# Kernel optimization log

Hardware: AMD Instinct MI355X
Metric: run time of the kernel (lower is better)

Reference implementation:

```python
import jax, jax.numpy as jnp
import numpy as np

B, T, E, H, L = 8, 4096, 1024, 16, 64  # batch, seq, embed, heads, local window
HD = E // H


def setup_inputs() -> dict:
    key = jax.random.key(0)
    ks = jax.random.split(key, 5)
    s = 1.0 / np.sqrt(E).astype(np.float32)
    x = jax.random.normal(ks[0], (B, T, E), dtype=jnp.float32)
    W_qkv = jax.random.normal(ks[1], (3 * E, E), dtype=jnp.float32) * s
    b_qkv = jnp.zeros((3 * E,), dtype=jnp.float32)
    W_out = jax.random.normal(ks[2], (E, E), dtype=jnp.float32) * s
    b_out = jnp.zeros((E,), dtype=jnp.float32)
    return {"x": x, "W_qkv": W_qkv, "b_qkv": b_qkv, "W_out": W_out, "b_out": b_out}


def reference(x, W_qkv, b_qkv, W_out, b_out):
    b, t, e = x.shape
    scaling = HD ** (-0.5)
    # T is already a multiple of L, so need_pad = 0 (matches torch path)
    qkv = x @ W_qkv.T + b_qkv                      # (B,T,3E)
    q, k, v = jnp.split(qkv, 3, axis=-1)           # each (B,T,E)
    q = q * scaling

    def to_blocks(a):
        # (B,T,E) -> (B,H,T/L,L,HD); matches torch view/transpose sequence
        return a.reshape(b, t, H, HD).transpose(0, 2, 1, 3).reshape(b, H, t // L, L, HD)

    qb, kb, vb = to_blocks(q), to_blocks(k), to_blocks(v)
    attn = jax.nn.softmax(jnp.einsum('bhnld,bhnmd->bhnlm', qb, kb), axis=-1)
    out = jnp.einsum('bhnlm,bhnmd->bhnld', attn, vb)  # (B,H,N,L,HD)
    out = out.reshape(b, H, t, HD).transpose(0, 2, 1, 3).reshape(b, t, e)
    return out @ W_out.T + b_out
```

## Files before the change

### kernel.cpp

```cpp
#include <hip/hip_runtime.h>
#include <hip/hip_bf16.h>

typedef __hip_bfloat16 bf16;
typedef __attribute__((ext_vector_type(8))) short short8;
typedef __attribute__((ext_vector_type(4))) float f32x4;

__device__ __forceinline__ void gload_lds16(const void* g, void* l) {
    __builtin_amdgcn_global_load_lds(
        (const __attribute__((address_space(1))) void*)g,
        (__attribute__((address_space(3))) void*)l, 16, 0, 0);
}

__device__ __forceinline__ void store_out(bf16* p, float v)  { *p = __float2bfloat16(v); }
__device__ __forceinline__ void store_out(float* p, float v) { *p = v; }

__global__ __launch_bounds__(256)
void cvt_f32_bf16(const float* __restrict__ in, bf16* __restrict__ out, long n)
{
    const long i = ((long)blockIdx.x * 256 + threadIdx.x) * 8;
    if (i + 8 > n) return;
    float4 a = *(const float4*)(in + i);
    float4 b = *(const float4*)(in + i + 4);
    bf16 o[8];
    o[0] = __float2bfloat16(a.x); o[1] = __float2bfloat16(a.y);
    o[2] = __float2bfloat16(a.z); o[3] = __float2bfloat16(a.w);
    o[4] = __float2bfloat16(b.x); o[5] = __float2bfloat16(b.y);
    o[6] = __float2bfloat16(b.z); o[7] = __float2bfloat16(b.w);
    *(uint4*)(out + i) = *(const uint4*)o;
}

template <typename OutT>
__global__ __launch_bounds__(512, 2)
void gemm256(const bf16* __restrict__ A, const bf16* __restrict__ Bt,
             const float* __restrict__ bias, OutT* __restrict__ C,
             int N, int K, int gxt)
{
    __shared__ bf16 As[4][8192];
    __shared__ bf16 Bs[4][8192];

    const int nwg  = gridDim.x;
    const int orig = blockIdx.x;
    const int qq = nwg >> 3, rr = nwg & 7, xc = orig & 7;
    const int wg = (xc < rr ? xc * (qq + 1) : rr * (qq + 1) + (xc - rr) * qq)
                 + (orig >> 3);
    const long m0 = (long)(wg / gxt) * 256;
    const long n0 = (long)(wg % gxt) * 256;

    const int tid = threadIdx.x;
    const int wv  = tid >> 6;
    const int ln  = tid & 63;
    const int l15 = ln & 15;
    const int qd  = ln >> 4;
    const int wm  = wv >> 2, wn = wv & 3;

    const int e0 = tid * 8;
    const int r0 = e0 >> 5, c0 = e0 & 31;
    const bf16* gA0 = A  + (m0 + r0) * K + c0;
    const bf16* gA1 = A  + (m0 + 128 + r0) * K + c0;
    const bf16* gB0 = Bt + (n0 + r0) * K + c0;
    const bf16* gB1 = Bt + (n0 + 128 + r0) * K + c0;
    const int lw = wv * 512;

    const int NT = K >> 5;

#define STAGE_A(bb, src) do { \
        gload_lds16(gA0 + (src) * 32, &As[bb][lw]); \
        gload_lds16(gA1 + (src) * 32, &As[bb][4096 + lw]); } while (0)
#define STAGE_B(bb, src) do { \
        gload_lds16(gB0 + (src) * 32, &Bs[bb][lw]); \
        gload_lds16(gB1 + (src) * 32, &Bs[bb][4096 + lw]); } while (0)

    {
        const int s1 = 1 < NT ? 1 : 0;
        const int s2 = 2 < NT ? 2 : 0;
        STAGE_A(0, 0);  STAGE_B(0, 0);
        STAGE_A(1, s1); STAGE_B(1, s1);
        STAGE_A(2, s2); STAGE_B(2, s2);
    }

    f32x4 acc[8][4] = {};

    for (int kt = 0; kt < NT; ++kt) {
        const int b   = kt & 3;
        const int ks  = kt + 3;
        const int bb  = ks & 3;
        const int src = ks < NT ? ks : 0;

        asm volatile("s_waitcnt vmcnt(8)" ::: "memory");
        __builtin_amdgcn_s_barrier();
        asm volatile("" ::: "memory");

        const bf16* Ab = As[b];
        const bf16* Bb = Bs[b];

        short8 af[4], bf[4];
#pragma unroll
        for (int mi = 0; mi < 4; ++mi)
            af[mi] = *(const short8*)&Ab[(wm * 128 + mi * 16 + l15) * 32 + qd * 8];
#pragma unroll
        for (int ni = 0; ni < 4; ++ni)
            bf[ni] = *(const short8*)&Bb[(wn * 64 + ni * 16 + l15) * 32 + qd * 8];
        STAGE_A(bb, src);
        __builtin_amdgcn_s_setprio(1);
#pragma unroll
        for (int mi = 0; mi < 4; ++mi)
#pragma unroll
            for (int ni = 0; ni < 4; ++ni)
                acc[mi][ni] = __builtin_amdgcn_mfma_f32_16x16x32_bf16(
                    af[mi], bf[ni], acc[mi][ni], 0, 0, 0);
        __builtin_amdgcn_s_setprio(0);

#pragma unroll
        for (int mi = 0; mi < 4; ++mi)
            af[mi] = *(const short8*)&Ab[(wm * 128 + (mi + 4) * 16 + l15) * 32 + qd * 8];
        STAGE_B(bb, src);
        __builtin_amdgcn_s_setprio(1);
#pragma unroll
        for (int mi = 0; mi < 4; ++mi)
#pragma unroll
            for (int ni = 0; ni < 4; ++ni)
                acc[mi + 4][ni] = __builtin_amdgcn_mfma_f32_16x16x32_bf16(
                    af[mi], bf[ni], acc[mi + 4][ni], 0, 0, 0);
        __builtin_amdgcn_s_setprio(0);
    }
#undef STAGE_A
#undef STAGE_B

    const long ccol = n0 + wn * 64;
    float bsv[4];
#pragma unroll
    for (int ni = 0; ni < 4; ++ni)
        bsv[ni] = bias[ccol + ni * 16 + l15];
#pragma unroll
    for (int mi = 0; mi < 8; ++mi) {
#pragma unroll
        for (int r = 0; r < 4; ++r) {
            const long row = m0 + wm * 128 + mi * 16 + qd * 4 + r;
            OutT* cp = C + row * N + ccol + l15;
#pragma unroll
            for (int ni = 0; ni < 4; ++ni)
                store_out(cp + ni * 16, acc[mi][ni][r] + bsv[ni]);
        }
    }
}

#define LROW 72

__global__ __launch_bounds__(256)
void attn_local(const bf16* __restrict__ qkv, bf16* __restrict__ out)
{
    __shared__ bf16 Qs[64 * LROW];
    __shared__ bf16 Ks[64 * LROW];
    __shared__ bf16 Vt[64 * LROW];
    __shared__ bf16 Ps[64 * LROW];

    const int cb = blockIdx.x;
    const int h  = blockIdx.y;
    const int tid = threadIdx.x;

    const long qoff = (long)cb * 64 * 3072 + h * 64;

#pragma unroll
    for (int p = 0; p < 2; ++p) {
        const int e = (p * 256 + tid) * 8;
        const int tk = e >> 6, cl = e & 63;
        const long g = qoff + (long)tk * 3072 + cl;
        *(uint4*)&Qs[tk * LROW + cl] = *(const uint4*)&qkv[g];
        *(uint4*)&Ks[tk * LROW + cl] = *(const uint4*)&qkv[g + 1024];
        uint4 vv = *(const uint4*)&qkv[g + 2048];
        const bf16* vp = (const bf16*)&vv;
#pragma unroll
        for (int j = 0; j < 8; ++j)
            Vt[(cl + j) * LROW + tk] = vp[j];
    }
    __syncthreads();

    const int wv = tid >> 6, ln = tid & 63, l15 = ln & 15, qd = ln >> 4;

    f32x4 sacc[4] = {};
#pragma unroll
    for (int kk = 0; kk < 64; kk += 32) {
        short8 aq = *(const short8*)&Qs[(wv * 16 + l15) * LROW + kk + qd * 8];
#pragma unroll
        for (int ni = 0; ni < 4; ++ni) {
            short8 bk = *(const short8*)&Ks[(ni * 16 + l15) * LROW + kk + qd * 8];
            sacc[ni] = __builtin_amdgcn_mfma_f32_16x16x32_bf16(aq, bk, sacc[ni], 0, 0, 0);
        }
    }

    float linv[4];
#pragma unroll
    for (int r = 0; r < 4; ++r) {
        float m = -3.4e38f;
#pragma unroll
        for (int ni = 0; ni < 4; ++ni) m = fmaxf(m, sacc[ni][r]);
#pragma unroll
        for (int off = 1; off < 16; off <<= 1) m = fmaxf(m, __shfl_xor(m, off));
        float s = 0.f, pv[4];
#pragma unroll
        for (int ni = 0; ni < 4; ++ni) {
            pv[ni] = __expf(0.125f * (sacc[ni][r] - m));
            s += pv[ni];
        }
#pragma unroll
        for (int off = 1; off < 16; off <<= 1) s += __shfl_xor(s, off);
        linv[r] = 1.f / s;
        const int row = wv * 16 + qd * 4 + r;
#pragma unroll
        for (int ni = 0; ni < 4; ++ni)
            Ps[row * LROW + ni * 16 + l15] = __float2bfloat16(pv[ni]);
    }
    __syncthreads();

    f32x4 oacc[4] = {};
#pragma unroll
    for (int kk = 0; kk < 64; kk += 32) {
        short8 ap = *(const short8*)&Ps[(wv * 16 + l15) * LROW + kk + qd * 8];
#pragma unroll
        for (int ni = 0; ni < 4; ++ni) {
            short8 bv = *(const short8*)&Vt[(ni * 16 + l15) * LROW + kk + qd * 8];
            oacc[ni] = __builtin_amdgcn_mfma_f32_16x16x32_bf16(ap, bv, oacc[ni], 0, 0, 0);
        }
    }

    const long obase = (long)cb * 64 * 1024 + h * 64;
#pragma unroll
    for (int r = 0; r < 4; ++r) {
        const int row = wv * 16 + qd * 4 + r;
#pragma unroll
        for (int ni = 0; ni < 4; ++ni)
            out[obase + (long)row * 1024 + ni * 16 + l15] =
                __float2bfloat16(oacc[ni][r] * linv[r]);
    }
}

extern "C" void kernel_launch(void* const* d_in, const int* in_sizes, int n_in,
                              void* d_out, int out_size, void* d_ws, size_t ws_size,
                              hipStream_t stream) {
    const float* x     = (const float*)d_in[0];
    const float* W_qkv = (const float*)d_in[1];
    const float* b_qkv = (const float*)d_in[2];
    const float* W_out = (const float*)d_in[3];
    const float* b_out = (const float*)d_in[4];
    float* out = (float*)d_out;

    bf16* Wqkv_b = (bf16*)d_ws;
    bf16* Wout_b = Wqkv_b + (size_t)3072 * 1024;
    bf16* chunk0 = Wout_b + (size_t)1024 * 1024;
    const size_t fixed_bytes = ((size_t)3072 * 1024 + (size_t)1024 * 1024) * 2;

    static const int cands[8] = {32768, 16384, 8192, 4096, 2048, 1024, 512, 256};
    int CH = 256;
    for (int i = 0; i < 8; ++i)
        if (fixed_bytes + (size_t)cands[i] * 10240 <= ws_size) { CH = cands[i]; break; }

    bf16* xb    = chunk0;
    bf16* qkvb  = xb + (size_t)CH * 1024;
    bf16* attnb = qkvb + (size_t)CH * 3072;

    const dim3 blk(256);
    const dim3 gblk(512);

    cvt_f32_bf16<<<dim3((3072 * 1024) / 2048), blk, 0, stream>>>(W_qkv, Wqkv_b, 3072 * 1024);
    cvt_f32_bf16<<<dim3((1024 * 1024) / 2048), blk, 0, stream>>>(W_out, Wout_b, 1024 * 1024);

    const int mt = CH / 256;

    for (int c0 = 0; c0 < 32768; c0 += CH) {
        const long ne = (long)CH * 1024;
        cvt_f32_bf16<<<dim3((int)(ne / 2048)), blk, 0, stream>>>(x + (size_t)c0 * 1024, xb, ne);
        gemm256<bf16><<<dim3(mt * (3072 / 256)), gblk, 0, stream>>>(
            xb, Wqkv_b, b_qkv, qkvb, 3072, 1024, 3072 / 256);
        attn_local<<<dim3(CH / 64, 16), blk, 0, stream>>>(qkvb, attnb);
        gemm256<float><<<dim3(mt * (1024 / 256)), gblk, 0, stream>>>(
            attnb, Wout_b, b_out, out + (size_t)c0 * 1024, 1024, 1024, 1024 / 256);
    }
}
```

Before: 576.6 us.

## Restructure GEMM mainloop with 64-wide K double buffer, swizzled LDS, fine barriers

The 256x256 GEMM mainloop moves from a 4-stage ring of 32-wide K slices to a double buffer of 64-wide K tiles split into two halves. The loop is hand-scheduled into half-tile MFMA chunks separated by barriers and sched_barriers so LDS reads, async global-to-LDS loads and MFMAs interleave more tightly. An XOR swizzle on the LDS column is added to reduce bank conflicts on the fragment reads. The extra barriers and the manual schedule may add sync overhead, and K must be a multiple of 128 for the unrolled loop.

```diff
diff --git a/kernel.cpp b/kernel.cpp
--- a/kernel.cpp
+++ b/kernel.cpp
@@ -35,8 +35,8 @@
              const float* __restrict__ bias, OutT* __restrict__ C,
              int N, int K, int gxt)
 {
-    __shared__ bf16 As[4][8192];
-    __shared__ bf16 Bs[4][8192];
+    __shared__ bf16 LA[2][2][8192];
+    __shared__ bf16 LB[2][2][8192];
 
     const int nwg  = gridDim.x;
     const int orig = blockIdx.x;
@@ -53,76 +53,75 @@
     const int qd  = ln >> 4;
     const int wm  = wv >> 2, wn = wv & 3;
 
-    const int e0 = tid * 8;
-    const int r0 = e0 >> 5, c0 = e0 & 31;
-    const bf16* gA0 = A  + (m0 + r0) * K + c0;
-    const bf16* gA1 = A  + (m0 + 128 + r0) * K + c0;
-    const bf16* gB0 = Bt + (n0 + r0) * K + c0;
-    const bf16* gB1 = Bt + (n0 + 128 + r0) * K + c0;
+    const int sl = (qd ^ (l15 & 3)) << 3;
+
+    const int srow = tid >> 2;
+    const int scol = ((tid & 3) ^ ((tid >> 2) & 3)) << 3;
+    const bf16* gA0 = A  + (m0 + srow) * K + scol;
+    const bf16* gA1 = A  + (m0 + 128 + srow) * K + scol;
+    const bf16* gB0 = Bt + (n0 + srow) * K + scol;
+    const bf16* gB1 = Bt + (n0 + 128 + srow) * K + scol;
     const int lw = wv * 512;
 
-    const int NT = K >> 5;
-
-#define STAGE_A(bb, src) do { \
-        gload_lds16(gA0 + (src) * 32, &As[bb][lw]); \
-        gload_lds16(gA1 + (src) * 32, &As[bb][4096 + lw]); } while (0)
-#define STAGE_B(bb, src) do { \
-        gload_lds16(gB0 + (src) * 32, &Bs[bb][lw]); \
-        gload_lds16(gB1 + (src) * 32, &Bs[bb][4096 + lw]); } while (0)
-
-    {
-        const int s1 = 1 < NT ? 1 : 0;
-        const int s2 = 2 < NT ? 2 : 0;
-        STAGE_A(0, 0);  STAGE_B(0, 0);
-        STAGE_A(1, s1); STAGE_B(1, s1);
-        STAGE_A(2, s2); STAGE_B(2, s2);
-    }
-
-    f32x4 acc[8][4] = {};
-
-    for (int kt = 0; kt < NT; ++kt) {
-        const int b   = kt & 3;
-        const int ks  = kt + 3;
-        const int bb  = ks & 3;
-        const int src = ks < NT ? ks : 0;
-
-        asm volatile("s_waitcnt vmcnt(8)" ::: "memory");
-        __builtin_amdgcn_s_barrier();
-        asm volatile("" ::: "memory");
-
-        const bf16* Ab = As[b];
-        const bf16* Bb = Bs[b];
-
-        short8 af[4], bf[4];
-#pragma unroll
-        for (int mi = 0; mi < 4; ++mi)
-            af[mi] = *(const short8*)&Ab[(wm * 128 + mi * 16 + l15) * 32 + qd * 8];
-#pragma unroll
-        for (int ni = 0; ni < 4; ++ni)
-            bf[ni] = *(const short8*)&Bb[(wn * 64 + ni * 16 + l15) * 32 + qd * 8];
-        STAGE_A(bb, src);
-        __builtin_amdgcn_s_setprio(1);
-#pragma unroll
-        for (int mi = 0; mi < 4; ++mi)
-#pragma unroll
-            for (int ni = 0; ni < 4; ++ni)
-                acc[mi][ni] = __builtin_amdgcn_mfma_f32_16x16x32_bf16(
-                    af[mi], bf[ni], acc[mi][ni], 0, 0, 0);
-        __builtin_amdgcn_s_setprio(0);
-
-#pragma unroll
-        for (int mi = 0; mi < 4; ++mi)
-            af[mi] = *(const short8*)&Ab[(wm * 128 + (mi + 4) * 16 + l15) * 32 + qd * 8];
-        STAGE_B(bb, src);
-        __builtin_amdgcn_s_setprio(1);
-#pragma unroll
-        for (int mi = 0; mi < 4; ++mi)
-#pragma unroll
-            for (int ni = 0; ni < 4; ++ni)
-                acc[mi + 4][ni] = __builtin_amdgcn_mfma_f32_16x16x32_bf16(
-                    af[mi], bf[ni], acc[mi + 4][ni], 0, 0, 0);
-        __builtin_amdgcn_s_setprio(0);
-    }
+    const int NT = K >> 6;
+
+#define STAGE_A(DB, KH, KT) do { \
+        gload_lds16(gA0 + (KT) * 64 + (KH) * 32, &LA[DB][KH][lw]); \
+        gload_lds16(gA1 + (KT) * 64 + (KH) * 32, &LA[DB][KH][4096 + lw]); } while (0)
+#define STAGE_B(DB, KH, KT) do { \
+        gload_lds16(gB0 + (KT) * 64 + (KH) * 32, &LB[DB][KH][lw]); \
+        gload_lds16(gB1 + (KT) * 64 + (KH) * 32, &LB[DB][KH][4096 + lw]); } while (0)
+
+    STAGE_A(0, 0, 0); STAGE_B(0, 0, 0);
+    STAGE_A(0, 1, 0); STAGE_B(0, 1, 0);
+    STAGE_A(1, 0, 1); STAGE_B(1, 0, 1);
+    asm volatile("s_waitcnt vmcnt(8)" ::: "memory");
+    __builtin_amdgcn_s_barrier();
+
+    f32x4 acc[2][4][4] = {};
+    short8 a[4], b[4];
+
+#define RD_B(DB, KH) \
+    _Pragma("unroll") \
+    for (int ni = 0; ni < 4; ++ni) \
+        b[ni] = *(const short8*)&LB[DB][KH][(wn * 64 + ni * 16 + l15) * 32 + sl];
+#define RD_A(DB, KH, CH) \
+    _Pragma("unroll") \
+    for (int mi = 0; mi < 4; ++mi) \
+        a[mi] = *(const short8*)&LA[DB][KH][(wm * 128 + (CH) * 64 + mi * 16 + l15) * 32 + sl];
+#define BARW() do { __builtin_amdgcn_s_barrier(); \
+        asm volatile("s_waitcnt lgkmcnt(0)" ::: "memory"); \
+        __builtin_amdgcn_sched_barrier(0); } while (0)
+#define MM(CH) do { __builtin_amdgcn_s_setprio(1); \
+        _Pragma("unroll") \
+        for (int mi = 0; mi < 4; ++mi) \
+            _Pragma("unroll") \
+            for (int ni = 0; ni < 4; ++ni) \
+                acc[CH][mi][ni] = __builtin_amdgcn_mfma_f32_16x16x32_bf16( \
+                    a[mi], b[ni], acc[CH][mi][ni], 0, 0, 0); \
+        __builtin_amdgcn_s_setprio(0); } while (0)
+#define BARP() __builtin_amdgcn_s_barrier()
+#define VM8BAR() do { asm volatile("s_waitcnt vmcnt(8)" ::: "memory"); \
+        __builtin_amdgcn_s_barrier(); } while (0)
+
+    for (int t = 0; t < NT; t += 2) {
+        const int s2 = (t + 2 < NT) ? t + 2 : 0;
+        const int s3 = (t + 3 < NT) ? t + 3 : 0;
+        RD_B(0, 0); RD_A(0, 0, 0); STAGE_A(1, 1, t + 1); BARW(); MM(0); BARP();
+        RD_A(0, 0, 1);             STAGE_B(1, 1, t + 1); BARW(); MM(1); VM8BAR();
+        RD_B(0, 1); RD_A(0, 1, 0); STAGE_A(0, 0, s2);    BARW(); MM(0); BARP();
+        RD_A(0, 1, 1);             STAGE_B(0, 0, s2);    BARW(); MM(1); VM8BAR();
+        RD_B(1, 0); RD_A(1, 0, 0); STAGE_A(0, 1, s2);    BARW(); MM(0); BARP();
+        RD_A(1, 0, 1);             STAGE_B(0, 1, s2);    BARW(); MM(1); VM8BAR();
+        RD_B(1, 1); RD_A(1, 1, 0); STAGE_A(1, 0, s3);    BARW(); MM(0); BARP();
+        RD_A(1, 1, 1);             STAGE_B(1, 0, s3);    BARW(); MM(1); VM8BAR();
+    }
+#undef RD_B
+#undef RD_A
+#undef BARW
+#undef MM
+#undef BARP
+#undef VM8BAR
 #undef STAGE_A
 #undef STAGE_B
 
@@ -132,14 +131,17 @@
     for (int ni = 0; ni < 4; ++ni)
         bsv[ni] = bias[ccol + ni * 16 + l15];
 #pragma unroll
-    for (int mi = 0; mi < 8; ++mi) {
-#pragma unroll
-        for (int r = 0; r < 4; ++r) {
-            const long row = m0 + wm * 128 + mi * 16 + qd * 4 + r;
-            OutT* cp = C + row * N + ccol + l15;
-#pragma unroll
-            for (int ni = 0; ni < 4; ++ni)
-                store_out(cp + ni * 16, acc[mi][ni][r] + bsv[ni]);
+    for (int ch = 0; ch < 2; ++ch) {
+#pragma unroll
+        for (int mi = 0; mi < 4; ++mi) {
+#pragma unroll
+            for (int r = 0; r < 4; ++r) {
+                const long row = m0 + wm * 128 + ch * 64 + mi * 16 + qd * 4 + r;
+                OutT* cp = C + row * N + ccol + l15;
+#pragma unroll
+                for (int ni = 0; ni < 4; ++ni)
+                    store_out(cp + ni * 16, acc[ch][mi][ni][r] + bsv[ni]);
+            }
         }
     }
 }
```

After: 613.0 us. +6.3%, slower.
